# Kernel optimization log

Measured on AMD Instinct MI355X. Metric: run time of the kernel, lower is better.

The kernel has to match this reference:

```python
import jax, jax.numpy as jnp
import numpy as np

B, IN_UNITS, IN_CHANNELS, NUM_UNITS, UNIT_SIZE = 256, 8, 1152, 10, 16
NUM_ITERS = 3


def setup_inputs() -> dict:
    key = jax.random.key(0)
    k1, k2 = jax.random.split(key)
    x = jax.random.normal(k1, (B, IN_UNITS, IN_CHANNELS), dtype=jnp.float32)
    # W from nn.Parameter(torch.randn(1, in_channels, num_units, unit_size, in_units)); drop leading 1
    W = jax.random.normal(k2, (IN_CHANNELS, NUM_UNITS, UNIT_SIZE, IN_UNITS), dtype=jnp.float32)
    return {"x": x, "W": W}


def reference(x, W):
    # x: [B, in_units=i, in_channels=j]; original transposes to [B, j, i]
    # u_hat = W @ x : [B, j, n, u]
    batch = x.shape[0]
    u_hat = jnp.einsum('jnui,bij->bjnu', W, x)
    b = jnp.zeros((IN_CHANNELS, NUM_UNITS), dtype=x.dtype)  # b_ij [j, n]
    v = None
    for _ in range(NUM_ITERS):
        # legacy F.softmax on 4D [1,j,n,1] -> dim=1 = in_channels axis
        c = jax.nn.softmax(b, axis=0)  # [j, n]
        s = jnp.einsum('jn,bjnu->bnu', c, u_hat)  # s_j: [B, n, u]
        # squash over dim=2 of [B,1,n,u,1] == num_units axis (axis=1 here)
        mag_sq = jnp.sum(s * s, axis=1, keepdims=True)  # [B, 1, u]
        v = (mag_sq / (1.0 + mag_sq)) * (s / jnp.sqrt(mag_sq))  # [B, n, u]
        # agreement: mean over batch of <u_hat, v>
        b = b + jnp.einsum('bjnu,bnu->jn', u_hat, v) / batch
    return v[..., None]  # [B, num_units, unit_size, 1] == v_j.squeeze(1)
```

## Files before the change

kernel.cpp:

```cpp
#include <hip/hip_runtime.h>
#include <stdint.h>

#define B   256
#define IU  8
#define JC  1152
#define NN  10
#define UU  16
#define NU  160
#define JN  11520
#define WROW 1280
#define NP  9216
#define KB  36

typedef short bf16x8 __attribute__((ext_vector_type(8)));
typedef float f32x4  __attribute__((ext_vector_type(4)));

__device__ __forceinline__ short f2bf(float f) {
    union { float f; uint32_t u; } cv; cv.f = f;
    uint32_t u = cv.u;
    uint32_t r = u + 0x7fffu + ((u >> 16) & 1u);
    return (short)(r >> 16);
}
__device__ __forceinline__ float bf2f(short h) {
    union { uint32_t u; float f; } cv; cv.u = ((uint32_t)(unsigned short)h) << 16;
    return cv.f;
}
__device__ __forceinline__ uint32_t bfbits(float f) {
    union { float f; uint32_t u; } cv; cv.f = f;
    return (cv.u + 0x7fffu + ((cv.u >> 16) & 1u)) >> 16;
}
__device__ __forceinline__ uint32_t pk2(float a, float b) {
    return bfbits(a) | (bfbits(b) << 16);
}
__device__ __forceinline__ void gload16(const void* g, void* l) {
    __builtin_amdgcn_global_load_lds(
        (const __attribute__((address_space(1))) void*)g,
        (__attribute__((address_space(3))) void*)l, 16, 0, 0);
}

__global__ void __launch_bounds__(256)
k_prep(const float* __restrict__ xg, const float* __restrict__ wg,
       short* __restrict__ wbf, short* __restrict__ xbf,
       float* __restrict__ expsum) {
    const int bid = blockIdx.x, tid = threadIdx.x;
    if (bid == 0 && tid < 32) expsum[tid] = 0.f;
    if (bid < 576) {
        const int jt = bid % 18, rt = bid / 18;
        const int j0 = jt * 64, r0 = rt * 64;
        __shared__ short T[64][72];
        #pragma unroll
        for (int p = 0; p < 4; ++p) {
            int idx = tid + 256 * p;
            int row = idx >> 4;
            int c4  = (idx & 15) * 4;
            float4 xv = *reinterpret_cast<const float4*>(
                &xg[(size_t)(r0 + row) * JC + j0 + c4]);
            T[c4+0][row] = f2bf(xv.x);
            T[c4+1][row] = f2bf(xv.y);
            T[c4+2][row] = f2bf(xv.z);
            T[c4+3][row] = f2bf(xv.w);
        }
        __syncthreads();
        #pragma unroll
        for (int p = 0; p < 2; ++p) {
            int idx = tid + 256 * p;
            int jl = idx >> 3;
            int r8 = (idx & 7) * 8;
            uint4 d = *reinterpret_cast<const uint4*>(&T[jl][r8]);
            *reinterpret_cast<uint4*>(&xbf[(size_t)(j0 + jl) * 2048 + r0 + r8]) = d;
        }
    } else {
        const int b2 = bid - 576;
        size_t base = (size_t)b2 * 2048 + (size_t)tid * 8;
        float4 f0 = *reinterpret_cast<const float4*>(&wg[base]);
        float4 f1 = *reinterpret_cast<const float4*>(&wg[base + 4]);
        uint4 d;
        d.x = pk2(f0.x, f0.y); d.y = pk2(f0.z, f0.w);
        d.z = pk2(f1.x, f1.y); d.w = pk2(f1.z, f1.w);
        *reinterpret_cast<uint4*>(&wbf[base]) = d;
    }
}

__global__ void __launch_bounds__(256, 2)
k_gemm1(const short* __restrict__ xbf, const short* __restrict__ wbf,
        float* __restrict__ s_part) {
    const int kb = blockIdx.x, mt = blockIdx.y;
    const int tid = threadIdx.x;
    const int wv = tid >> 6, lane = tid & 63;
    const int q = lane >> 4, l16 = lane & 15;
    const int b0 = mt * 32;
    const int jb0 = kb * 32;
    const int mfrag = wv >> 1;
    const int ntb = (wv & 1) * 5;

    __shared__ __align__(16) short As[8 * 32 * 8];
    __shared__ __align__(16) short Bs[8 * 160 * 8];

    f32x4 acc[5];
    #pragma unroll
    for (int nt = 0; nt < 5; ++nt) acc[nt] = (f32x4){0.f, 0.f, 0.f, 0.f};

    for (int jc = 0; jc < 4; ++jc) {
        const int j0 = jb0 + jc * 8;
        __syncthreads();
        gload16(xbf + ((size_t)(j0 + (tid >> 5)) * 2048 + (size_t)(b0 + (tid & 31)) * 8),
                &As[tid * 8]);
        const short* wsrc = wbf + (size_t)j0 * WROW;
        #pragma unroll
        for (int p = 0; p < 5; ++p) {
            int ridx = tid + 256 * p;
            gload16(wsrc + (size_t)ridx * 8, &Bs[ridx * 8]);
        }
        __syncthreads();
        #pragma unroll
        for (int s = 0; s < 2; ++s) {
            int jj = s * 4 + q;
            bf16x8 av = *reinterpret_cast<const bf16x8*>(
                &As[(jj * 32 + mfrag * 16 + l16) << 3]);
            #pragma unroll
            for (int nt = 0; nt < 5; ++nt) {
                bf16x8 bv = *reinterpret_cast<const bf16x8*>(
                    &Bs[(jj * 160 + (ntb + nt) * 16 + l16) << 3]);
                acc[nt] = __builtin_amdgcn_mfma_f32_16x16x32_bf16(av, bv, acc[nt], 0, 0, 0);
            }
        }
    }
    float* dst = s_part + (size_t)(kb * 8 + mt) * 5120;
    #pragma unroll
    for (int nt = 0; nt < 5; ++nt)
        #pragma unroll
        for (int reg = 0; reg < 4; ++reg)
            dst[(mfrag * 16 + q * 4 + reg) * 160 + (ntb + nt) * 16 + l16] = acc[nt][reg];
}

__global__ void __launch_bounds__(320, 2)
k_reduce_s(const float* __restrict__ s_part, float* __restrict__ vdst,
           const float* __restrict__ expsum, int t0) {
    const int b = blockIdx.x, tid = threadIdx.x;
    const int t = tid % 160, kq = tid / 160;
    const int mt = b >> 5, bl = b & 31;
    const size_t off = (size_t)mt * 5120 + bl * 160 + t;

    __shared__ float invn[NN];
    if (tid < NN) invn[tid] = t0 ? (1.f / (float)JC) : 1.f / expsum[tid];

    float s = 0.f;
    for (int r = 0; r < 18; ++r)
        s += s_part[(size_t)(kq * 18 + r) * 40960 + off];

    __shared__ float red[2][160];
    __shared__ float sv[NU];
    __shared__ float fb[UU];
    red[kq][t] = s;
    __syncthreads();
    if (tid < NU) sv[tid] = (red[0][tid] + red[1][tid]) * invn[tid >> 4];
    __syncthreads();
    if (tid < UU) {
        float m = 0.f;
        #pragma unroll
        for (int n = 0; n < NN; ++n) { float z = sv[n*16 + tid]; m = fmaf(z, z, m); }
        fb[tid] = sqrtf(m) / (1.f + m);
    }
    __syncthreads();
    if (tid < NU)
        vdst[(size_t)b * NU + tid] = sv[tid] * fb[tid & 15];
}

__global__ void __launch_bounds__(256)
k_route(const float* __restrict__ vg, const float* __restrict__ xg,
        const float* __restrict__ wg, float* __restrict__ blog,
        short* __restrict__ wbf, float* __restrict__ expsum, int t0) {
    const int jt = blockIdx.x, ng = blockIdx.y;
    const int j0 = jt * 32, n0 = ng * 2, m0 = n0 * 16;
    const int tid = threadIdx.x;
    const int wv = tid >> 6, lane = tid & 63;
    const int q = lane >> 4, l16 = lane & 15;
    const int mtl = wv >> 1, ntc = wv & 1;

    __shared__ __align__(16) short Ash[8192], Asl[8192];
    __shared__ __align__(16) short Bsh[8192], Bsl[8192];
    __shared__ float Gt[32 * 32];
    __shared__ float red[256];
    __shared__ float esh[64];

    #pragma unroll
    for (int p = 0; p < 32; ++p) {
        int e = tid + 256 * p;
        int b = e >> 5, ml = e & 31;
        float vv = vg[(size_t)b * NU + m0 + ml];
        short hi = f2bf(vv);
        short lo = f2bf(vv - bf2f(hi));
        int a = (b >> 6) * 2048 + (((b >> 3) & 7) * 32 + ml) * 8 + (b & 7);
        Ash[a] = hi; Asl[a] = lo;
    }

    float part = 0.f;
    for (int i = 0; i < 8; ++i) {
        __syncthreads();
        #pragma unroll
        for (int p = 0; p < 32; ++p) {
            int e = tid + 256 * p;
            int b = e >> 5, jl = e & 31;
            float xv = xg[(size_t)b * NP + i * JC + j0 + jl];
            short hi = f2bf(xv);
            short lo = f2bf(xv - bf2f(hi));
            int a = (b >> 6) * 2048 + (((b >> 3) & 7) * 32 + jl) * 8 + (b & 7);
            Bsh[a] = hi; Bsl[a] = lo;
        }
        __syncthreads();
        f32x4 acc = (f32x4){0.f, 0.f, 0.f, 0.f};
        #pragma unroll
        for (int ks = 0; ks < 4; ++ks)
            #pragma unroll
            for (int s = 0; s < 2; ++s) {
                int kc = s * 4 + q;
                const int ai = ks * 2048 + (kc * 32 + mtl * 16 + l16) * 8;
                const int bi = ks * 2048 + (kc * 32 + ntc * 16 + l16) * 8;
                bf16x8 ah = *reinterpret_cast<const bf16x8*>(&Ash[ai]);
                bf16x8 al = *reinterpret_cast<const bf16x8*>(&Asl[ai]);
                bf16x8 bh = *reinterpret_cast<const bf16x8*>(&Bsh[bi]);
                bf16x8 bl = *reinterpret_cast<const bf16x8*>(&Bsl[bi]);
                acc = __builtin_amdgcn_mfma_f32_16x16x32_bf16(ah, bh, acc, 0, 0, 0);
                acc = __builtin_amdgcn_mfma_f32_16x16x32_bf16(ah, bl, acc, 0, 0, 0);
                acc = __builtin_amdgcn_mfma_f32_16x16x32_bf16(al, bh, acc, 0, 0, 0);
            }
        __syncthreads();
        #pragma unroll
        for (int r = 0; r < 4; ++r)
            Gt[(mtl * 16 + q * 4 + r) * 32 + ntc * 16 + l16] = acc[r];
        __syncthreads();
        {
            int jl = tid & 31, rr = tid >> 5;
            int nn = rr >> 2, uq = rr & 3;
            const float* wrow = wg + (size_t)(j0 + jl) * WROW + (n0 + nn) * 128 + i;
            #pragma unroll
            for (int k = 0; k < 4; ++k)
                part = fmaf(Gt[(nn * 16 + uq * 4 + k) * 32 + jl],
                            wrow[(uq * 4 + k) * 8], part);
        }
    }
    {
        int jl = tid & 31, rr = tid >> 5;
        red[((rr >> 2) * 32 + jl) * 4 + (rr & 3)] = part;
    }
    __syncthreads();
    if (tid < 64) {
        int jl = tid & 31, nn = tid >> 5;
        int ri = (nn * 32 + jl) * 4;
        float d = (red[ri] + red[ri + 1] + red[ri + 2] + red[ri + 3])
                  * (1.f / (float)B);
        int bi = (j0 + jl) * NN + n0 + nn;
        float nb = t0 ? d : (blog[bi] + d);
        blog[bi] = nb;
        float e = __expf(nb);
        esh[jl * 2 + nn] = e;
        float ssum = e;
        ssum += __shfl_xor(ssum, 1);  ssum += __shfl_xor(ssum, 2);
        ssum += __shfl_xor(ssum, 4);  ssum += __shfl_xor(ssum, 8);
        ssum += __shfl_xor(ssum, 16);
        if ((tid & 31) == 0) atomicAdd(&expsum[n0 + nn], ssum);
    }
    __syncthreads();
    {
        int row = tid >> 3, seg = tid & 7;
        float e = esh[row * 2 + (seg >> 2)];
        const float4* wp = reinterpret_cast<const float4*>(
            wg + (size_t)(j0 + row) * WROW + n0 * 128 + seg * 32);
        short* dst = wbf + (size_t)(j0 + row) * WROW + n0 * 128 + seg * 32;
        #pragma unroll
        for (int k2 = 0; k2 < 4; ++k2) {
            float4 f0 = wp[k2 * 2], f1 = wp[k2 * 2 + 1];
            uint4 dd;
            dd.x = pk2(f0.x * e, f0.y * e); dd.y = pk2(f0.z * e, f0.w * e);
            dd.z = pk2(f1.x * e, f1.y * e); dd.w = pk2(f1.z * e, f1.w * e);
            *reinterpret_cast<uint4*>(&dst[k2 * 8]) = dd;
        }
    }
}

extern "C" void kernel_launch(void* const* d_in, const int* in_sizes, int n_in,
                              void* d_out, int out_size, void* d_ws, size_t ws_size,
                              hipStream_t stream) {
    const float* x = (const float*)d_in[0];
    const float* w = (const float*)d_in[1];
    float* out = (float*)d_out;

    float* ws     = (float*)d_ws;
    float* blog   = ws;
    float* expsum = blog + JN;
    float* v      = expsum + 32;
    short* wbf    = (short*)(v + (size_t)B * NU);
    short* xbf    = wbf + (size_t)JC * WROW;
    float* s_part = (float*)(xbf + (size_t)JC * 2048);

    k_prep<<<1296, 256, 0, stream>>>(x, w, wbf, xbf, expsum);
    for (int t = 0; t < 3; ++t) {
        k_gemm1<<<dim3(KB, 8), 256, 0, stream>>>(xbf, wbf, s_part);
        k_reduce_s<<<B, 320, 0, stream>>>(
            s_part, (t == 2) ? out : v,
            expsum + ((t == 0) ? 0 : (t - 1) * 16), (t == 0) ? 1 : 0);
        if (t < 2)
            k_route<<<dim3(36, 5), 256, 0, stream>>>(
                v, x, w, blog, wbf, expsum + t * 16, (t == 0) ? 1 : 0);
    }
}
```

Before: 142.6 us.

## Vectorize route staging loads, XOR-swizzle LDS tiles, and double gemm1 K-chunk

In k_route, the v and x staging loads now use float4 reads: each thread loads a contiguous run of x for one batch row instead of strided scalar loads. The LDS A/B tiles use an XOR swizzle of the column index with kc, which avoids bank conflicts on the 16-byte MFMA fragment reads. In k_gemm1, each K-chunk is now 16 channels instead of 8, which halves the number of barrier-separated load/compute phases. The costs are more LDS per block in gemm1, which may reduce occupancy, and x reads in route that are less coalesced across threads, since each thread walks a different batch row.

New measurement: 153.0 us. 7.3% more time.

```diff
diff --git a/kernel.cpp b/kernel.cpp
--- a/kernel.cpp
+++ b/kernel.cpp
@@ -93,27 +93,32 @@
     const int mfrag = wv >> 1;
     const int ntb = (wv & 1) * 5;
 
-    __shared__ __align__(16) short As[8 * 32 * 8];
-    __shared__ __align__(16) short Bs[8 * 160 * 8];
+    __shared__ __align__(16) short As[16 * 32 * 8];
+    __shared__ __align__(16) short Bs[16 * 160 * 8];
 
     f32x4 acc[5];
     #pragma unroll
     for (int nt = 0; nt < 5; ++nt) acc[nt] = (f32x4){0.f, 0.f, 0.f, 0.f};
 
-    for (int jc = 0; jc < 4; ++jc) {
-        const int j0 = jb0 + jc * 8;
-        __syncthreads();
-        gload16(xbf + ((size_t)(j0 + (tid >> 5)) * 2048 + (size_t)(b0 + (tid & 31)) * 8),
-                &As[tid * 8]);
+    for (int jc = 0; jc < 2; ++jc) {
+        const int j0 = jb0 + jc * 16;
+        __syncthreads();
+        #pragma unroll
+        for (int p = 0; p < 2; ++p) {
+            int idx = tid + 256 * p;
+            gload16(xbf + ((size_t)(j0 + (idx >> 5)) * 2048
+                           + (size_t)(b0 + (idx & 31)) * 8),
+                    &As[idx * 8]);
+        }
         const short* wsrc = wbf + (size_t)j0 * WROW;
         #pragma unroll
-        for (int p = 0; p < 5; ++p) {
+        for (int p = 0; p < 10; ++p) {
             int ridx = tid + 256 * p;
             gload16(wsrc + (size_t)ridx * 8, &Bs[ridx * 8]);
         }
         __syncthreads();
         #pragma unroll
-        for (int s = 0; s < 2; ++s) {
+        for (int s = 0; s < 4; ++s) {
             int jj = s * 4 + q;
             bf16x8 av = *reinterpret_cast<const bf16x8*>(
                 &As[(jj * 32 + mfrag * 16 + l16) << 3]);
@@ -184,28 +189,46 @@
     __shared__ float esh[64];
 
     #pragma unroll
-    for (int p = 0; p < 32; ++p) {
-        int e = tid + 256 * p;
-        int b = e >> 5, ml = e & 31;
-        float vv = vg[(size_t)b * NU + m0 + ml];
-        short hi = f2bf(vv);
-        short lo = f2bf(vv - bf2f(hi));
-        int a = (b >> 6) * 2048 + (((b >> 3) & 7) * 32 + ml) * 8 + (b & 7);
-        Ash[a] = hi; Asl[a] = lo;
+    for (int p = 0; p < 8; ++p) {
+        int idx = tid + 256 * p;
+        int b = idx >> 3, c4 = (idx & 7) * 4;
+        float4 vv = *reinterpret_cast<const float4*>(&vg[(size_t)b * NU + m0 + c4]);
+        int kc = (b >> 3) & 7;
+        int abase = (b >> 6) * 2048 + kc * 256 + (b & 7);
+        #pragma unroll
+        for (int e = 0; e < 4; ++e) {
+            float f = (e == 0) ? vv.x : (e == 1) ? vv.y : (e == 2) ? vv.z : vv.w;
+            short hi = f2bf(f);
+            short lo = f2bf(f - bf2f(hi));
+            int a = abase + (((c4 + e) ^ kc) << 3);
+            Ash[a] = hi; Asl[a] = lo;
+        }
     }
 
     float part = 0.f;
+    const int jl_c = tid & 31, rr = tid >> 5;
+    const int nn_c = rr >> 2, uq = rr & 3;
+
     for (int i = 0; i < 8; ++i) {
         __syncthreads();
-        #pragma unroll
-        for (int p = 0; p < 32; ++p) {
-            int e = tid + 256 * p;
-            int b = e >> 5, jl = e & 31;
-            float xv = xg[(size_t)b * NP + i * JC + j0 + jl];
-            short hi = f2bf(xv);
-            short lo = f2bf(xv - bf2f(hi));
-            int a = (b >> 6) * 2048 + (((b >> 3) & 7) * 32 + jl) * 8 + (b & 7);
-            Bsh[a] = hi; Bsl[a] = lo;
+        {
+            int b = tid;
+            const float4* xp = reinterpret_cast<const float4*>(
+                &xg[(size_t)b * NP + i * JC + j0]);
+            int kc = (b >> 3) & 7;
+            int abase = (b >> 6) * 2048 + kc * 256 + (b & 7);
+            #pragma unroll
+            for (int c = 0; c < 8; ++c) {
+                float4 xv = xp[c];
+                #pragma unroll
+                for (int e = 0; e < 4; ++e) {
+                    float f = (e == 0) ? xv.x : (e == 1) ? xv.y : (e == 2) ? xv.z : xv.w;
+                    short hi = f2bf(f);
+                    short lo = f2bf(f - bf2f(hi));
+                    int a = abase + (((c * 4 + e) ^ kc) << 3);
+                    Bsh[a] = hi; Bsl[a] = lo;
+                }
+            }
         }
         __syncthreads();
         f32x4 acc = (f32x4){0.f, 0.f, 0.f, 0.f};
@@ -214,8 +237,10 @@
             #pragma unroll
             for (int s = 0; s < 2; ++s) {
                 int kc = s * 4 + q;
-                const int ai = ks * 2048 + (kc * 32 + mtl * 16 + l16) * 8;
-                const int bi = ks * 2048 + (kc * 32 + ntc * 16 + l16) * 8;
+                const int ai = ks * 2048 + kc * 256
+                             + (((mtl * 16 + l16) ^ kc) << 3);
+                const int bi = ks * 2048 + kc * 256
+                             + (((ntc * 16 + l16) ^ kc) << 3);
                 bf16x8 ah = *reinterpret_cast<const bf16x8*>(&Ash[ai]);
                 bf16x8 al = *reinterpret_cast<const bf16x8*>(&Asl[ai]);
                 bf16x8 bh = *reinterpret_cast<const bf16x8*>(&Bsh[bi]);
@@ -230,19 +255,15 @@
             Gt[(mtl * 16 + q * 4 + r) * 32 + ntc * 16 + l16] = acc[r];
         __syncthreads();
         {
-            int jl = tid & 31, rr = tid >> 5;
-            int nn = rr >> 2, uq = rr & 3;
-            const float* wrow = wg + (size_t)(j0 + jl) * WROW + (n0 + nn) * 128 + i;
+            const float* wrow = wg + (size_t)(j0 + jl_c) * WROW
+                              + (n0 + nn_c) * 128 + i;
             #pragma unroll
             for (int k = 0; k < 4; ++k)
-                part = fmaf(Gt[(nn * 16 + uq * 4 + k) * 32 + jl],
+                part = fmaf(Gt[(nn_c * 16 + uq * 4 + k) * 32 + jl_c],
                             wrow[(uq * 4 + k) * 8], part);
         }
     }
-    {
-        int jl = tid & 31, rr = tid >> 5;
-        red[((rr >> 2) * 32 + jl) * 4 + (rr & 3)] = part;
-    }
+    red[((rr >> 2) * 32 + jl_c) * 4 + (rr & 3)] = part;
     __syncthreads();
     if (tid < 64) {
         int jl = tid & 31, nn = tid >> 5;
```
